# Performance work log

Hardware: AMD Instinct MI355X
Metric: run time of the kernel (lower is better)

The kernel has to match this reference:

```python
import jax, jax.numpy as jnp
import numpy as np

OUT_H = 8      # hardcoded transformer output height in the source
MAX_W = 384    # hardcoded max_width pad target
MAX_ROI = 10   # hardcoded max_roi_num


def _warp_one(fm, theta, w):
    # fm: [H, W, C]; theta: [2, 3] affine; w: scalar int box width (<= MAX_W)
    H, W, C = fm.shape
    dt = fm.dtype
    y_t = jnp.linspace(-1.0, 1.0, OUT_H).astype(dt)[:, None]        # [8, 1]
    j = jnp.arange(MAX_W, dtype=dt)[None, :]                        # [1, 384]
    denom = jnp.maximum(w - 1, 1).astype(dt)
    x_t = -1.0 + 2.0 * j / denom                                    # linspace(-1,1,w) padded out to 384
    # affine sampling grid (STN): source normalized coords
    xs = theta[0, 0] * x_t + theta[0, 1] * y_t + theta[0, 2]        # [8, 384]
    ys = theta[1, 0] * x_t + theta[1, 1] * y_t + theta[1, 2]
    # map from [-1, 1] to pixel coords (DeepMind STN convention)
    x = (xs + 1.0) * jnp.asarray(W, dt) * 0.5
    y = (ys + 1.0) * jnp.asarray(H, dt) * 0.5
    x0f = jnp.floor(x); y0f = jnp.floor(y)
    x0 = jnp.clip(x0f.astype(jnp.int32), 0, W - 1)
    x1 = jnp.clip(x0f.astype(jnp.int32) + 1, 0, W - 1)
    y0 = jnp.clip(y0f.astype(jnp.int32), 0, H - 1)
    y1 = jnp.clip(y0f.astype(jnp.int32) + 1, 0, H - 1)
    Ia = fm[y0, x0]; Ib = fm[y1, x0]; Ic = fm[y0, x1]; Id = fm[y1, x1]  # [8,384,C]
    wa = ((x0f + 1.0 - x) * (y0f + 1.0 - y))[..., None]
    wb = ((x0f + 1.0 - x) * (y - y0f))[..., None]
    wc = ((x - x0f) * (y0f + 1.0 - y))[..., None]
    wd = ((x - x0f) * (y - y0f))[..., None]
    out = wa * Ia + wb * Ib + wc * Ic + wd * Id                     # [8, 384, C]
    # crop_and_resize with full box [0,0,1,1] to the same [8,w] size is identity;
    # pad_to_bounding_box(0,0,8,384) == zero out columns >= w
    mask = (jnp.arange(MAX_W) < w)[None, :, None]
    return jnp.where(mask, out, jnp.zeros((), dt))


def setup_inputs() -> dict:
    key = jax.random.key(0)
    k1, k2, k3, k4 = jax.random.split(key, 4)
    B, H, W, C = 8, 160, 160, 256
    feature_map = jax.random.normal(k1, (B, H, W, C), dtype=jnp.float32)
    transform_matrixs = jax.random.uniform(k2, (MAX_ROI, 6), dtype=jnp.float32)
    box_masks = jax.random.randint(k3, (MAX_ROI,), 0, B, dtype=jnp.int32)
    box_widths = jax.random.randint(k4, (MAX_ROI,), 32, MAX_W, dtype=jnp.int32)
    return {"feature_map": feature_map, "transform_matrixs": transform_matrixs,
            "box_masks": box_masks, "box_widths": box_widths}


def reference(feature_map, transform_matrixs, box_masks, box_widths):
    # per-box gather of the source image in the batch
    fms = jnp.take(feature_map, box_masks, axis=0)          # [10, H, W, C]
    thetas = transform_matrixs.reshape(-1, 2, 3)            # [10, 2, 3]
    rois = jax.vmap(_warp_one)(fms, thetas, box_widths)     # [10, 8, 384, C]
    return rois
```

## Files before the change

### kernel.cpp

```cpp
#include <hip/hip_runtime.h>
#include <stdint.h>

#define OUT_H 8
#define MAX_W 384
#define MAX_ROI 10
#define FH 160
#define FW 160
#define FC 256

__global__ __launch_bounds__(256) void roi_warp_kernel(
    const float* __restrict__ fm,
    const float* __restrict__ theta,
    const int* __restrict__ masks,
    const int* __restrict__ widths,
    float* __restrict__ out)
{
    const int tx = threadIdx.x;
    const int cg = tx & 63;
    const int jj = tx >> 6;
    int b = blockIdx.x;
    const int jt = b % 96;
    b /= 96;
    const int i   = b & 7;
    const int roi = b >> 3;
    const int j = jt * 4 + jj;
    const int c = cg << 2;

    const int w = widths[roi];
    float* outp = out + ((((size_t)roi * OUT_H + i) * MAX_W + j) * FC + c);

    if (j >= w) {
        float4 z = make_float4(0.f, 0.f, 0.f, 0.f);
        *reinterpret_cast<float4*>(outp) = z;
        return;
    }

    const int bidx = masks[roi];
    const float* tp = theta + roi * 6;
    const float t00 = tp[0];
    const float t01 = tp[1];
    const float t02 = tp[2];
    const float t10 = tp[3];
    const float t11 = tp[4];
    const float t12 = tp[5];

    const int wm1 = (w - 1) > 1 ? (w - 1) : 1;
    const float denom = (float)wm1;
    const float x_t = -1.0f + 2.0f * (float)j / denom;
    const float y_t = -1.0f + 2.0f * (float)i / 7.0f;

    const float xs = t00 * x_t + t01 * y_t + t02;
    const float ys = t10 * x_t + t11 * y_t + t12;
    const float x = (xs + 1.0f) * ((float)FW * 0.5f);
    const float y = (ys + 1.0f) * ((float)FH * 0.5f);

    const float x0f = floorf(x);
    const float y0f = floorf(y);
    int x0 = (int)x0f;
    int y0 = (int)y0f;
    int x1 = x0 + 1;
    int y1 = y0 + 1;
    x0 = min(max(x0, 0), FW - 1);
    x1 = min(max(x1, 0), FW - 1);
    y0 = min(max(y0, 0), FH - 1);
    y1 = min(max(y1, 0), FH - 1);

    const float gx0 = (x0f + 1.0f) - x;
    const float gx1 = x - x0f;
    const float gy0 = (y0f + 1.0f) - y;
    const float gy1 = y - y0f;
    const float wa = gx0 * gy0;
    const float wb = gx0 * gy1;
    const float wc = gx1 * gy0;
    const float wd = gx1 * gy1;

    const size_t plane = (size_t)bidx * ((size_t)FH * FW * FC);
    const float* pA = fm + plane + (((size_t)y0 * FW + x0) * FC + c);
    const float* pB = fm + plane + (((size_t)y1 * FW + x0) * FC + c);
    const float* pC = fm + plane + (((size_t)y0 * FW + x1) * FC + c);
    const float* pD = fm + plane + (((size_t)y1 * FW + x1) * FC + c);

    const float4 A = *reinterpret_cast<const float4*>(pA);
    const float4 B = *reinterpret_cast<const float4*>(pB);
    const float4 C = *reinterpret_cast<const float4*>(pC);
    const float4 D = *reinterpret_cast<const float4*>(pD);

    float4 R;
    R.x = wa * A.x + wb * B.x + wc * C.x + wd * D.x;
    R.y = wa * A.y + wb * B.y + wc * C.y + wd * D.y;
    R.z = wa * A.z + wb * B.z + wc * C.z + wd * D.z;
    R.w = wa * A.w + wb * B.w + wc * C.w + wd * D.w;

    *reinterpret_cast<float4*>(outp) = R;
}

extern "C" void kernel_launch(void* const* d_in, const int* in_sizes, int n_in,
                              void* d_out, int out_size, void* d_ws, size_t ws_size,
                              hipStream_t stream) {
    const float* fm     = (const float*)d_in[0];
    const float* theta  = (const float*)d_in[1];
    const int*   masks  = (const int*)d_in[2];
    const int*   widths = (const int*)d_in[3];
    float*       out    = (float*)d_out;

    const int grid = MAX_ROI * OUT_H * (MAX_W / 4);
    roi_warp_kernel<<<grid, 256, 0, stream>>>(fm, theta, masks, widths, out);
}
```

Before: 248.7 us.

## Process four columns per thread with nontemporal stores and XCD-aware block remap

Each thread now handles four output columns instead of one, so the grid is cut by a factor of four and the theta and row setup is amortized. Output writes use nontemporal stores to avoid polluting cache with the large write-only result. Block IDs are permuted so consecutive blocks on the same XCD cover contiguous work, which should improve L2 locality for the gathered feature-map rows. Fewer blocks and more serial work per thread may reduce latency hiding on the gathers.

```diff
diff --git a/kernel.cpp b/kernel.cpp
--- a/kernel.cpp
+++ b/kernel.cpp
@@ -8,6 +8,12 @@
 #define FW 160
 #define FC 256
 
+#define JPB 16
+#define JT (MAX_W / JPB)
+#define NBLK (MAX_ROI * OUT_H * JT)
+
+typedef float v4f __attribute__((ext_vector_type(4)));
+
 __global__ __launch_bounds__(256) void roi_warp_kernel(
     const float* __restrict__ fm,
     const float* __restrict__ theta,
@@ -15,83 +21,80 @@
     const int* __restrict__ widths,
     float* __restrict__ out)
 {
-    const int tx = threadIdx.x;
-    const int cg = tx & 63;
-    const int jj = tx >> 6;
-    int b = blockIdx.x;
-    const int jt = b % 96;
-    b /= 96;
-    const int i   = b & 7;
-    const int roi = b >> 3;
-    const int j = jt * 4 + jj;
-    const int c = cg << 2;
+    const int tx   = threadIdx.x;
+    const int lane = tx & 63;
+    const int wg   = tx >> 6;
+    const int c    = lane << 2;
+
+    const int bid = blockIdx.x;
+    const int wid = (bid & 7) * (NBLK / 8) + (bid >> 3);
+    const int roi = wid / (OUT_H * JT);
+    const int rem = wid - roi * (OUT_H * JT);
+    const int i   = rem / JT;
+    const int jt  = rem - i * JT;
+
+    const int j0 = jt * JPB + wg * 4;
 
     const int w = widths[roi];
-    float* outp = out + ((((size_t)roi * OUT_H + i) * MAX_W + j) * FC + c);
+    float* outp = out + ((((size_t)roi * OUT_H + i) * MAX_W + j0) * FC + c);
 
-    if (j >= w) {
-        float4 z = make_float4(0.f, 0.f, 0.f, 0.f);
-        *reinterpret_cast<float4*>(outp) = z;
+    if (j0 >= w) {
+        const v4f z = (v4f){0.f, 0.f, 0.f, 0.f};
+        #pragma unroll
+        for (int u = 0; u < 4; ++u)
+            __builtin_nontemporal_store(z, reinterpret_cast<v4f*>(outp + (size_t)u * FC));
         return;
     }
 
     const int bidx = masks[roi];
     const float* tp = theta + roi * 6;
-    const float t00 = tp[0];
-    const float t01 = tp[1];
-    const float t02 = tp[2];
-    const float t10 = tp[3];
-    const float t11 = tp[4];
-    const float t12 = tp[5];
+    const float t00 = tp[0], t01 = tp[1], t02 = tp[2];
+    const float t10 = tp[3], t11 = tp[4], t12 = tp[5];
 
     const int wm1 = (w - 1) > 1 ? (w - 1) : 1;
-    const float denom = (float)wm1;
-    const float x_t = -1.0f + 2.0f * (float)j / denom;
+    const float rd2 = 2.0f / (float)wm1;
     const float y_t = -1.0f + 2.0f * (float)i / 7.0f;
+    const float xs_y = t01 * y_t + t02;
+    const float ys_y = t11 * y_t + t12;
 
-    const float xs = t00 * x_t + t01 * y_t + t02;
-    const float ys = t10 * x_t + t11 * y_t + t12;
-    const float x = (xs + 1.0f) * ((float)FW * 0.5f);
-    const float y = (ys + 1.0f) * ((float)FH * 0.5f);
+    const float* plane = fm + (size_t)bidx * ((size_t)FH * FW * FC) + c;
 
-    const float x0f = floorf(x);
-    const float y0f = floorf(y);
-    int x0 = (int)x0f;
-    int y0 = (int)y0f;
-    int x1 = x0 + 1;
-    int y1 = y0 + 1;
-    x0 = min(max(x0, 0), FW - 1);
-    x1 = min(max(x1, 0), FW - 1);
-    y0 = min(max(y0, 0), FH - 1);
-    y1 = min(max(y1, 0), FH - 1);
+    #pragma unroll
+    for (int u = 0; u < 4; ++u) {
+        const int j = j0 + u;
+        v4f R = (v4f){0.f, 0.f, 0.f, 0.f};
+        if (j < w) {
+            const float x_t = fmaf((float)j, rd2, -1.0f);
+            const float x = (fmaf(t00, x_t, xs_y) + 1.0f) * ((float)FW * 0.5f);
+            const float y = (fmaf(t10, x_t, ys_y) + 1.0f) * ((float)FH * 0.5f);
 
-    const float gx0 = (x0f + 1.0f) - x;
-    const float gx1 = x - x0f;
-    const float gy0 = (y0f + 1.0f) - y;
-    const float gy1 = y - y0f;
-    const float wa = gx0 * gy0;
-    const float wb = gx0 * gy1;
-    const float wc = gx1 * gy0;
-    const float wd = gx1 * gy1;
+            const float x0f = floorf(x);
+            const float y0f = floorf(y);
+            int x0 = (int)x0f, y0 = (int)y0f;
+            int x1 = x0 + 1,   y1 = y0 + 1;
+            x0 = min(max(x0, 0), FW - 1);
+            x1 = min(max(x1, 0), FW - 1);
+            y0 = min(max(y0, 0), FH - 1);
+            y1 = min(max(y1, 0), FH - 1);
 
-    const size_t plane = (size_t)bidx * ((size_t)FH * FW * FC);
-    const float* pA = fm + plane + (((size_t)y0 * FW + x0) * FC + c);
-    const float* pB = fm + plane + (((size_t)y1 * FW + x0) * FC + c);
-    const float* pC = fm + plane + (((size_t)y0 * FW + x1) * FC + c);
-    const float* pD = fm + plane + (((size_t)y1 * FW + x1) * FC + c);
+            const float gx0 = (x0f + 1.0f) - x;
+            const float gx1 = x - x0f;
+            const float gy0 = (y0f + 1.0f) - y;
+            const float gy1 = y - y0f;
+            const float wa = gx0 * gy0;
+            const float wb = gx0 * gy1;
+            const float wc = gx1 * gy0;
+            const float wd = gx1 * gy1;
 
-    const float4 A = *reinterpret_cast<const float4*>(pA);
-    const float4 B = *reinterpret_cast<const float4*>(pB);
-    const float4 C = *reinterpret_cast<const float4*>(pC);
-    const float4 D = *reinterpret_cast<const float4*>(pD);
+            const v4f A  = *reinterpret_cast<const v4f*>(plane + ((size_t)y0 * FW + x0) * FC);
+            const v4f Bv = *reinterpret_cast<const v4f*>(plane + ((size_t)y1 * FW + x0) * FC);
+            const v4f Cv = *reinterpret_cast<const v4f*>(plane + ((size_t)y0 * FW + x1) * FC);
+            const v4f Dv = *reinterpret_cast<const v4f*>(plane + ((size_t)y1 * FW + x1) * FC);
 
-    float4 R;
-    R.x = wa * A.x + wb * B.x + wc * C.x + wd * D.x;
-    R.y = wa * A.y + wb * B.y + wc * C.y + wd * D.y;
-    R.z = wa * A.z + wb * B.z + wc * C.z + wd * D.z;
-    R.w = wa * A.w + wb * B.w + wc * C.w + wd * D.w;
-
-    *reinterpret_cast<float4*>(outp) = R;
+            R = wa * A + wb * Bv + wc * Cv + wd * Dv;
+        }
+        __builtin_nontemporal_store(R, reinterpret_cast<v4f*>(outp + (size_t)u * FC));
+    }
 }
 
 extern "C" void kernel_launch(void* const* d_in, const int* in_sizes, int n_in,
@@ -103,6 +106,5 @@
     const int*   widths = (const int*)d_in[3];
     float*       out    = (float*)d_out;
 
-    const int grid = MAX_ROI * OUT_H * (MAX_W / 4);
-    roi_warp_kernel<<<grid, 256, 0, stream>>>(fm, theta, masks, widths, out);
+    roi_warp_kernel<<<NBLK, 256, 0, stream>>>(fm, theta, masks, widths, out);
 }
```

Measured after the change: 256.4 us. +3.1%, slower.
